# Kernel optimization log

Measured on AMD Instinct MI355X. Metric: run time of the kernel, lower is better.

Reference implementation:

```python
import jax, jax.numpy as jnp
import numpy as np

SIZE, D, DLOC, NUM_LABELS = 784, 32, 2, 10
LABEL_SITE = SIZE // 2
INIT_STD = 0.01


def tree_contract(mats):
    # mats: [n, B, D, D]; binary-tree pairwise matmul matching the torch loop
    # (odd level: last matrix set aside, re-appended after the pairwise bmm)
    n = mats.shape[0]
    while n > 1:
        if n % 2 == 1:
            lone = mats[-1:]
            mats = mats[:-1]
        else:
            lone = None
        mats = jnp.einsum('nbij,nbjk->nbik', mats[0::2], mats[1::2])
        if lone is not None:
            mats = jnp.concatenate([mats, lone], axis=0)
        n = mats.shape[0]
    return mats[0]  # [B, D, D]


def setup_inputs() -> dict:
    key = jax.random.key(0)
    k1, k2, k3 = jax.random.split(key, 3)
    batch_input = jax.random.uniform(k1, (128, SIZE), dtype=jnp.float32)
    # 'random_eye' init: identity (broadcast over site / physical / label dims) + noise
    core_tensors = (jnp.broadcast_to(jnp.eye(D, dtype=jnp.float32)[None, :, :, None],
                                     (SIZE, D, D, DLOC))
                    + INIT_STD * jax.random.normal(k2, (SIZE, D, D, DLOC), dtype=jnp.float32))
    label_tensor = (jnp.broadcast_to(jnp.eye(D, dtype=jnp.float32)[:, :, None],
                                     (D, D, NUM_LABELS))
                    + INIT_STD * jax.random.normal(k3, (D, D, NUM_LABELS), dtype=jnp.float32))
    return {"batch_input": batch_input, "core_tensors": core_tensors,
            "label_tensor": label_tensor}


def reference(batch_input, core_tensors, label_tensor):
    # embed: x -> [1-x, x], shape [B, S, d]
    embedded = jnp.stack([1.0 - batch_input, batch_input], axis=-1)
    # contract each core with its local feature vector -> [S, B, D, D]
    batch_mats = jnp.einsum('sijd,bsd->sbij', core_tensors, embedded)
    left = tree_contract(batch_mats[:LABEL_SITE])    # [B, D, D]
    right = tree_contract(batch_mats[LABEL_SITE:])   # [B, D, D]
    # trace(left @ label_l @ right) per batch and label -> [B, num_labels]
    scores = jnp.einsum('bij,jkl,bki->bl', left, label_tensor, right)
    return scores
```

## Files before the change

### kernel.cpp

```cpp
#include <hip/hip_runtime.h>
#include <cstddef>


typedef short bfrag __attribute__((ext_vector_type(4)));
typedef float facc  __attribute__((ext_vector_type(4)));

#if !defined(__HIP_DEVICE_COMPILE__)
#define MFMA16(a, b, c) (c)
#elif __has_builtin(__builtin_amdgcn_mfma_f32_16x16x16bf16_1k)
#define MFMA16(a, b, c) __builtin_amdgcn_mfma_f32_16x16x16bf16_1k(a, b, c, 0, 0, 0)
#elif __has_builtin(__builtin_amdgcn_mfma_f32_16x16x16_bf16)
#define MFMA16(a, b, c) __builtin_amdgcn_mfma_f32_16x16x16_bf16(a, b, c, 0, 0, 0)
#else
#error "no 16x16x16 bf16 MFMA builtin on this target"
#endif

#define CORE2_FLOATS (784 * 2048)

__device__ __forceinline__ short bf16h(float v) {
  unsigned u = __float_as_uint(v) + 0x8000u;
  return (short)(u >> 16);
}

__device__ __forceinline__ bfrag pack4(const facc v) {
  bfrag r;
#pragma unroll
  for (int j = 0; j < 4; ++j) r[j] = bf16h(v[j]);
  return r;
}

__device__ __forceinline__ void split4(const float* v, bfrag& hi, bfrag& lo) {
#pragma unroll
  for (int j = 0; j < 4; ++j) {
    unsigned u = (__float_as_uint(v[j]) + 0x8000u) & 0xFFFF0000u;
    hi[j] = (short)(u >> 16);
    float lf = v[j] - __uint_as_float(u);
    lo[j] = bf16h(lf);
  }
}

__global__ __launch_bounds__(256) void xform_k(const float* __restrict__ core,
                                               float* __restrict__ core2) {
  const int s = blockIdx.x;
  const int tid = threadIdx.x;
  const float4* src = (const float4*)(core + (size_t)s * 2048);
  float4* dst = (float4*)(core2 + (size_t)s * 2048);
#pragma unroll
  for (int u = 0; u < 2; ++u) {
    int o = tid + 256 * u;
    int lane = o & 63;
    int f = o >> 6;
    int p = f & 1;
    int h2 = (f >> 1) & 1;
    int r = f >> 2;
    int col16 = lane & 15;
    int q = lane >> 4;
    dst[o] = src[(16 * r + col16) * 16 + 8 * h2 + 2 * q + p];
  }
}

__device__ __forceinline__ void site_update(facc (&acc)[2][2],
                                            const float4 (&raw)[2][2][2],
                                            float xv, const float (&ds)[4]) {
  bfrag B[2][2];
#pragma unroll
  for (int h2 = 0; h2 < 2; ++h2)
#pragma unroll
    for (int c = 0; c < 2; ++c) B[h2][c] = pack4(acc[h2][c]);

  bfrag A[2][2];
#pragma unroll
  for (int r = 0; r < 2; ++r)
#pragma unroll
    for (int h2 = 0; h2 < 2; ++h2) {
      float4 f0 = raw[r][h2][0];
      float4 f1 = raw[r][h2][1];
      float e0 = f0.x + xv * (f0.y - f0.x);
      float e1 = f0.z + xv * (f0.w - f0.z);
      float e2 = f1.x + xv * (f1.y - f1.x);
      float e3 = f1.z + xv * (f1.w - f1.z);
      if (r == h2) { e0 -= ds[0]; e1 -= ds[1]; e2 -= ds[2]; e3 -= ds[3]; }
      bfrag a; a[0] = bf16h(e0); a[1] = bf16h(e1); a[2] = bf16h(e2); a[3] = bf16h(e3);
      A[r][h2] = a;
    }

#pragma unroll
  for (int r = 0; r < 2; ++r)
#pragma unroll
    for (int c = 0; c < 2; ++c) {
      acc[r][c] = MFMA16(A[r][0], B[0][c], acc[r][c]);
      acc[r][c] = MFMA16(A[r][1], B[1][c], acc[r][c]);
    }
}

__global__ __launch_bounds__(128, 8) void seg_mfma(const float* __restrict__ x,
                                                   const float* __restrict__ core2,
                                                   float* __restrict__ seg) {
  const int lane = threadIdx.x & 63;
  const int w = threadIdx.x >> 6;
  const int col16 = lane & 15;
  const int q = lane >> 4;

  const int bid = blockIdx.x;
  const int c2 = bid & 7;
  const int g = (bid >> 3) & 63;
  const int c1 = bid >> 9;
  const int combo = c1 * 8 + c2;
  const int h = combo >> 4;
  const int t = combo & 15;
  const int b = g * 2 + w;

  const int start = (t < 8) ? 25 * t : 200 + 24 * (t - 8);
  const int len = (t < 8) ? 25 : 24;
  const int s_lo = h * 392 + start;
  const int s_hi = s_lo + len - 1;

  float ds[4];
#pragma unroll
  for (int j = 0; j < 4; ++j) ds[j] = (4 * q + j == col16) ? 1.0f : 0.0f;

  facc acc[2][2];
#pragma unroll
  for (int r = 0; r < 2; ++r)
#pragma unroll
    for (int c = 0; c < 2; ++c)
#pragma unroll
      for (int j = 0; j < 4; ++j)
        acc[r][c][j] = (16 * r + 4 * q + j == 16 * c + col16) ? 1.0f : 0.0f;

  const float4* cp = (const float4*)core2;
  const float* xb = x + b * 784;

  for (int s = s_hi; s >= s_lo; --s) {
    const size_t sb = (size_t)s * 512;
    float4 raw[2][2][2];
#pragma unroll
    for (int r = 0; r < 2; ++r)
#pragma unroll
      for (int h2 = 0; h2 < 2; ++h2)
#pragma unroll
        for (int p = 0; p < 2; ++p)
          raw[r][h2][p] = cp[sb + ((r * 2 + h2) * 2 + p) * 64 + lane];
    const float xv = xb[s];
    site_update(acc, raw, xv, ds);
  }

  float4* o = (float4*)(seg + (size_t)((b * 2 + h) * 16 + t) * 1024);
#pragma unroll
  for (int R = 0; R < 2; ++R)
#pragma unroll
    for (int H = 0; H < 2; ++H)
      o[(R * 2 + H) * 64 + lane] =
          make_float4(acc[H][R][0], acc[H][R][1], acc[H][R][2], acc[H][R][3]);
}

__device__ __forceinline__ void fold_step(facc (&acc)[2][2], const float4 (&av)[2][2]) {
  bfrag Ahi[2][2], Alo[2][2], Bhi[2][2], Blo[2][2];
#pragma unroll
  for (int R = 0; R < 2; ++R)
#pragma unroll
    for (int H = 0; H < 2; ++H) {
      float v[4] = {av[R][H].x, av[R][H].y, av[R][H].z, av[R][H].w};
      split4(v, Ahi[R][H], Alo[R][H]);
    }
#pragma unroll
  for (int H = 0; H < 2; ++H)
#pragma unroll
    for (int c = 0; c < 2; ++c) {
      float v[4] = {acc[H][c][0], acc[H][c][1], acc[H][c][2], acc[H][c][3]};
      split4(v, Bhi[H][c], Blo[H][c]);
    }
  facc n[2][2];
#pragma unroll
  for (int R = 0; R < 2; ++R)
#pragma unroll
    for (int c = 0; c < 2; ++c) {
      facc z;
#pragma unroll
      for (int j = 0; j < 4; ++j) z[j] = 0.0f;
#pragma unroll
      for (int H = 0; H < 2; ++H) {
        z = MFMA16(Ahi[R][H], Bhi[H][c], z);
        z = MFMA16(Ahi[R][H], Blo[H][c], z);
        z = MFMA16(Alo[R][H], Bhi[H][c], z);
      }
      n[R][c] = z;
    }
#pragma unroll
  for (int R = 0; R < 2; ++R)
#pragma unroll
    for (int c = 0; c < 2; ++c) acc[R][c] = n[R][c];
}

__global__ __launch_bounds__(256) void finish_k(const float* __restrict__ seg,
                                                const float* __restrict__ label,
                                                float* __restrict__ out) {
  const int tid = threadIdx.x;
  const int lane = tid & 63;
  const int wv = tid >> 6;
  const int side = wv >> 1;
  const int half = wv & 1;
  const int b = blockIdx.x;
  const int chain = 2 * b + side;
  const int col16 = lane & 15;
  const int q = lane >> 4;

  __shared__ float smX[2][32 * 36];
  __shared__ float smF[1024];
  __shared__ float red[40];

  facc acc[2][2];
#pragma unroll
  for (int r = 0; r < 2; ++r)
#pragma unroll
    for (int c = 0; c < 2; ++c)
#pragma unroll
      for (int j = 0; j < 4; ++j)
        acc[r][c][j] = (16 * r + 4 * q + j == 16 * c + col16) ? 1.0f : 0.0f;

  const float* base = seg + (size_t)(chain * 16) * 1024;
  const int t0 = half * 8;

  float4 av[2][2];
#pragma unroll
  for (int R = 0; R < 2; ++R)
#pragma unroll
    for (int H = 0; H < 2; ++H)
      av[R][H] = *(const float4*)&base[(size_t)t0 * 1024 + ((R * 2 + H) * 64 + lane) * 4];
  for (int t = t0; t < t0 + 7; ++t) {
    float4 nav[2][2];
#pragma unroll
    for (int R = 0; R < 2; ++R)
#pragma unroll
      for (int H = 0; H < 2; ++H)
        nav[R][H] =
            *(const float4*)&base[(size_t)(t + 1) * 1024 + ((R * 2 + H) * 64 + lane) * 4];
    fold_step(acc, av);
#pragma unroll
    for (int R = 0; R < 2; ++R)
#pragma unroll
      for (int H = 0; H < 2; ++H) av[R][H] = nav[R][H];
  }
  fold_step(acc, av);

  if (half == 1) {
#pragma unroll
    for (int r = 0; r < 2; ++r)
#pragma unroll
      for (int c = 0; c < 2; ++c)
#pragma unroll
        for (int j = 0; j < 4; ++j)
          smX[side][(16 * r + 4 * q + j) * 36 + 16 * c + col16] = acc[r][c][j];
  }
  __syncthreads();
  if (half == 0) {
    float4 qv[2][2];
#pragma unroll
    for (int R = 0; R < 2; ++R)
#pragma unroll
      for (int H = 0; H < 2; ++H)
        qv[R][H] = *(const float4*)&smX[side][(16 * R + col16) * 36 + 16 * H + 4 * q];
    fold_step(acc, qv);
  }
  __syncthreads();

  if (wv == 0) {
#pragma unroll
    for (int r = 0; r < 2; ++r)
#pragma unroll
      for (int c = 0; c < 2; ++c)
#pragma unroll
        for (int j = 0; j < 4; ++j)
          smX[0][(16 * r + 4 * q + j) * 36 + 16 * c + col16] = acc[r][c][j];
  }
  __syncthreads();
  if (wv == 2) {
    float4 qv[2][2];
#pragma unroll
    for (int R = 0; R < 2; ++R)
#pragma unroll
      for (int H = 0; H < 2; ++H)
        qv[R][H] = *(const float4*)&smX[0][(16 * R + col16) * 36 + 16 * H + 4 * q];
    fold_step(acc, qv);
#pragma unroll
    for (int r = 0; r < 2; ++r)
#pragma unroll
      for (int c = 0; c < 2; ++c)
#pragma unroll
        for (int j = 0; j < 4; ++j)
          smF[(16 * r + 4 * q + j) * 32 + 16 * c + col16] = acc[r][c][j];
  }
  __syncthreads();

  float part[10];
#pragma unroll
  for (int l = 0; l < 10; ++l) part[l] = 0.0f;
#pragma unroll
  for (int u = 0; u < 4; ++u) {
    int e = tid + 256 * u;
    float v = smF[e];
    const float* lb = label + (size_t)e * 10;
#pragma unroll
    for (int l = 0; l < 10; ++l) part[l] += v * lb[l];
  }
#pragma unroll
  for (int l = 0; l < 10; ++l) {
#pragma unroll
    for (int o = 32; o > 0; o >>= 1) part[l] += __shfl_xor(part[l], o, 64);
  }
  if (lane == 0) {
#pragma unroll
    for (int l = 0; l < 10; ++l) red[wv * 10 + l] = part[l];
  }
  __syncthreads();
  if (tid < 10) {
    float s = 0.0f;
#pragma unroll
    for (int v = 0; v < 4; ++v) s += red[v * 10 + tid];
    out[b * 10 + tid] = s;
  }
}

extern "C" void kernel_launch(void* const* d_in, const int* in_sizes, int n_in,
                              void* d_out, int out_size, void* d_ws, size_t ws_size,
                              hipStream_t stream) {
  const float* x = (const float*)d_in[0];
  const float* core = (const float*)d_in[1];
  const float* label = (const float*)d_in[2];
  float* out = (float*)d_out;
  float* ws = (float*)d_ws;

  float* core2 = ws;
  float* seg = ws + CORE2_FLOATS;

  hipLaunchKernelGGL(xform_k, dim3(784), dim3(256), 0, stream, core, core2);
  hipLaunchKernelGGL(seg_mfma, dim3(2048), dim3(128), 0, stream, x, core2, seg);
  hipLaunchKernelGGL(finish_k, dim3(128), dim3(256), 0, stream, seg, label, out);
}
```

Before: 104.2 us.

## Pre-pack core tensors as bf16 base/delta pairs and widen segment blocks

The transform kernel now precomputes each core element as a packed bf16 pair: the embedding base (with the identity subtracted) and the delta between the two physical slices. This halves the per-site bytes the segment kernel reads and reduces the per-element embedding to a single fma. The segment kernel also moves from 2 to 4 waves per block, so each block covers four batch rows and the grid has half as many blocks. The cost is extra bf16 rounding on the delta term, which may shift accuracy slightly.

Result: faster. 95.74 us (-8.1%).

```diff
diff --git a/kernel.cpp b/kernel.cpp
--- a/kernel.cpp
+++ b/kernel.cpp
@@ -15,7 +15,7 @@
 #error "no 16x16x16 bf16 MFMA builtin on this target"
 #endif
 
-#define CORE2_FLOATS (784 * 2048)
+#define CORE2B_DWORDS (784 * 1024)
 
 __device__ __forceinline__ short bf16h(float v) {
   unsigned u = __float_as_uint(v) + 0x8000u;
@@ -40,61 +40,40 @@
 }
 
 __global__ __launch_bounds__(256) void xform_k(const float* __restrict__ core,
-                                               float* __restrict__ core2) {
+                                               unsigned* __restrict__ core2b) {
   const int s = blockIdx.x;
   const int tid = threadIdx.x;
-  const float4* src = (const float4*)(core + (size_t)s * 2048);
-  float4* dst = (float4*)(core2 + (size_t)s * 2048);
-#pragma unroll
-  for (int u = 0; u < 2; ++u) {
-    int o = tid + 256 * u;
-    int lane = o & 63;
-    int f = o >> 6;
-    int p = f & 1;
-    int h2 = (f >> 1) & 1;
-    int r = f >> 2;
-    int col16 = lane & 15;
-    int q = lane >> 4;
-    dst[o] = src[(16 * r + col16) * 16 + 8 * h2 + 2 * q + p];
-  }
-}
-
-__device__ __forceinline__ void site_update(facc (&acc)[2][2],
-                                            const float4 (&raw)[2][2][2],
-                                            float xv, const float (&ds)[4]) {
-  bfrag B[2][2];
-#pragma unroll
-  for (int h2 = 0; h2 < 2; ++h2)
-#pragma unroll
-    for (int c = 0; c < 2; ++c) B[h2][c] = pack4(acc[h2][c]);
-
-  bfrag A[2][2];
-#pragma unroll
-  for (int r = 0; r < 2; ++r)
-#pragma unroll
-    for (int h2 = 0; h2 < 2; ++h2) {
-      float4 f0 = raw[r][h2][0];
-      float4 f1 = raw[r][h2][1];
-      float e0 = f0.x + xv * (f0.y - f0.x);
-      float e1 = f0.z + xv * (f0.w - f0.z);
-      float e2 = f1.x + xv * (f1.y - f1.x);
-      float e3 = f1.z + xv * (f1.w - f1.z);
-      if (r == h2) { e0 -= ds[0]; e1 -= ds[1]; e2 -= ds[2]; e3 -= ds[3]; }
-      bfrag a; a[0] = bf16h(e0); a[1] = bf16h(e1); a[2] = bf16h(e2); a[3] = bf16h(e3);
-      A[r][h2] = a;
+  const int f = tid >> 6;
+  const int lane = tid & 63;
+  const int col16 = lane & 15;
+  const int q = lane >> 4;
+  const int r = f >> 1;
+  const int h2 = f & 1;
+  const int i = 16 * r + col16;
+  const int c0 = 16 * h2 + 4 * q;
+
+  const float* src = core + (size_t)s * 2048 + ((size_t)i * 32 + c0) * 2;
+  float4 v0 = *(const float4*)(src);
+  float4 v1 = *(const float4*)(src + 4);
+
+  unsigned w[4];
+  {
+    float m0[4] = {v0.x, v0.z, v1.x, v1.z};
+    float m1[4] = {v0.y, v0.w, v1.y, v1.w};
+#pragma unroll
+    for (int j = 0; j < 4; ++j) {
+      float e0 = m0[j] - ((i == c0 + j) ? 1.0f : 0.0f);
+      float d = m1[j] - m0[j];
+      w[j] = ((unsigned)(unsigned short)bf16h(d) << 16) |
+             (unsigned)(unsigned short)bf16h(e0);
     }
-
-#pragma unroll
-  for (int r = 0; r < 2; ++r)
-#pragma unroll
-    for (int c = 0; c < 2; ++c) {
-      acc[r][c] = MFMA16(A[r][0], B[0][c], acc[r][c]);
-      acc[r][c] = MFMA16(A[r][1], B[1][c], acc[r][c]);
-    }
-}
-
-__global__ __launch_bounds__(128, 8) void seg_mfma(const float* __restrict__ x,
-                                                   const float* __restrict__ core2,
+  }
+  *(uint4*)(core2b + (size_t)s * 1024 + (size_t)tid * 4) =
+      make_uint4(w[0], w[1], w[2], w[3]);
+}
+
+__global__ __launch_bounds__(256, 4) void seg_mfma(const float* __restrict__ x,
+                                                   const unsigned* __restrict__ core2b,
                                                    float* __restrict__ seg) {
   const int lane = threadIdx.x & 63;
   const int w = threadIdx.x >> 6;
@@ -103,22 +82,18 @@
 
   const int bid = blockIdx.x;
   const int c2 = bid & 7;
-  const int g = (bid >> 3) & 63;
-  const int c1 = bid >> 9;
+  const int g = (bid >> 3) & 31;
+  const int c1 = bid >> 8;
   const int combo = c1 * 8 + c2;
   const int h = combo >> 4;
   const int t = combo & 15;
-  const int b = g * 2 + w;
+  const int b = g * 4 + w;
 
   const int start = (t < 8) ? 25 * t : 200 + 24 * (t - 8);
   const int len = (t < 8) ? 25 : 24;
   const int s_lo = h * 392 + start;
   const int s_hi = s_lo + len - 1;
 
-  float ds[4];
-#pragma unroll
-  for (int j = 0; j < 4; ++j) ds[j] = (4 * q + j == col16) ? 1.0f : 0.0f;
-
   facc acc[2][2];
 #pragma unroll
   for (int r = 0; r < 2; ++r)
@@ -128,21 +103,45 @@
       for (int j = 0; j < 4; ++j)
         acc[r][c][j] = (16 * r + 4 * q + j == 16 * c + col16) ? 1.0f : 0.0f;
 
-  const float4* cp = (const float4*)core2;
+  const uint4* cp = (const uint4*)core2b;
   const float* xb = x + b * 784;
 
   for (int s = s_hi; s >= s_lo; --s) {
-    const size_t sb = (size_t)s * 512;
-    float4 raw[2][2][2];
-#pragma unroll
-    for (int r = 0; r < 2; ++r)
-#pragma unroll
-      for (int h2 = 0; h2 < 2; ++h2)
-#pragma unroll
-        for (int p = 0; p < 2; ++p)
-          raw[r][h2][p] = cp[sb + ((r * 2 + h2) * 2 + p) * 64 + lane];
+    uint4 raw[4];
+#pragma unroll
+    for (int f = 0; f < 4; ++f) raw[f] = cp[(size_t)s * 256 + f * 64 + lane];
     const float xv = xb[s];
-    site_update(acc, raw, xv, ds);
+
+    bfrag B[2][2];
+#pragma unroll
+    for (int h2 = 0; h2 < 2; ++h2)
+#pragma unroll
+      for (int c = 0; c < 2; ++c) B[h2][c] = pack4(acc[h2][c]);
+
+    bfrag A[2][2];
+#pragma unroll
+    for (int r = 0; r < 2; ++r)
+#pragma unroll
+      for (int h2 = 0; h2 < 2; ++h2) {
+        unsigned wd[4] = {raw[r * 2 + h2].x, raw[r * 2 + h2].y, raw[r * 2 + h2].z,
+                          raw[r * 2 + h2].w};
+        bfrag a;
+#pragma unroll
+        for (int j = 0; j < 4; ++j) {
+          float e0 = __uint_as_float(wd[j] << 16);
+          float d = __uint_as_float(wd[j] & 0xFFFF0000u);
+          a[j] = bf16h(fmaf(xv, d, e0));
+        }
+        A[r][h2] = a;
+      }
+
+#pragma unroll
+    for (int r = 0; r < 2; ++r)
+#pragma unroll
+      for (int c = 0; c < 2; ++c) {
+        acc[r][c] = MFMA16(A[r][0], B[0][c], acc[r][c]);
+        acc[r][c] = MFMA16(A[r][1], B[1][c], acc[r][c]);
+      }
   }
 
   float4* o = (float4*)(seg + (size_t)((b * 2 + h) * 16 + t) * 1024);
@@ -328,12 +327,11 @@
   const float* core = (const float*)d_in[1];
   const float* label = (const float*)d_in[2];
   float* out = (float*)d_out;
-  float* ws = (float*)d_ws;
-
-  float* core2 = ws;
-  float* seg = ws + CORE2_FLOATS;
-
-  hipLaunchKernelGGL(xform_k, dim3(784), dim3(256), 0, stream, core, core2);
-  hipLaunchKernelGGL(seg_mfma, dim3(2048), dim3(128), 0, stream, x, core2, seg);
+
+  unsigned* core2b = (unsigned*)d_ws;
+  float* seg = (float*)d_ws + CORE2B_DWORDS;
+
+  hipLaunchKernelGGL(xform_k, dim3(784), dim3(256), 0, stream, core, core2b);
+  hipLaunchKernelGGL(seg_mfma, dim3(1024), dim3(256), 0, stream, x, core2b, seg);
   hipLaunchKernelGGL(finish_k, dim3(128), dim3(256), 0, stream, seg, label, out);
 }
```
